# Performance work log

Measured on AMD Instinct MI355X. Metric: run time of the kernel, lower is better.

Reference implementation:

```python
import jax, jax.numpy as jnp
import numpy as np

N = 100000        # number of nodes
E = 3200000       # number of edges (avg degree 32)
D_IN = 128
D_OUT = 128


def setup_inputs() -> dict:
    key = jax.random.key(0)
    k_x, k_src, k_dst, k_w, k_W, k_b = jax.random.split(key, 6)
    x = jax.random.normal(k_x, (N, D_IN), dtype=jnp.float32)
    edge_src = jax.random.randint(k_src, (E,), 0, N, dtype=jnp.int32)
    edge_dst = jnp.sort(jax.random.randint(k_dst, (E,), 0, N, dtype=jnp.int32))
    edge_weight = jax.random.uniform(k_w, (E,), dtype=jnp.float32)
    # Linear params, init uniform(-stdv, stdv) with stdv = 1/sqrt(in_features)
    stdv = 1.0 / np.sqrt(D_IN)
    W = jax.random.uniform(k_W, (D_IN, D_OUT), dtype=jnp.float32, minval=-stdv, maxval=stdv)
    b = jax.random.uniform(k_b, (D_OUT,), dtype=jnp.float32, minval=-stdv, maxval=stdv)
    return {"x": x, "W": W, "b": b, "edge_weight": edge_weight,
            "edge_src": edge_src, "edge_dst": edge_dst}


def reference(x, W, b, edge_weight, edge_src, edge_dst):
    # support = W(input)  -- dense projection [N, D_OUT]
    support = x @ W + b
    # output = spmm(adj, support): out[dst] += w_e * support[src]
    msgs = support[edge_src] * edge_weight[:, None]          # [E, D_OUT]
    out = jax.ops.segment_sum(msgs, edge_dst, num_segments=x.shape[0])
    return out
```

## Files before the change

kernel.cpp:

```cpp
#include <hip/hip_runtime.h>

#define D 128

typedef unsigned short u16;
typedef __attribute__((ext_vector_type(8))) short bf16x8;
typedef __attribute__((ext_vector_type(4))) float f32x4;

__device__ __forceinline__ u16 f32_to_bf16(float f) {
    unsigned u = __float_as_uint(f);
    unsigned rounding = 0x7fffu + ((u >> 16) & 1u);
    return (u16)((u + rounding) >> 16);
}

__device__ __forceinline__ float bf16_to_f32(u16 s) {
    return __uint_as_float(((unsigned)s) << 16);
}

__global__ __launch_bounds__(256) void prep_kernel(
    const float* __restrict__ W, u16* __restrict__ Wt)
{
    int idx = blockIdx.x * 256 + threadIdx.x;
    int n = idx >> 7;
    int k = idx & 127;
    Wt[idx] = f32_to_bf16(W[k * 128 + n]);
}

__global__ __launch_bounds__(256) void gemm_mfma_kernel(
    const float* __restrict__ x, const u16* __restrict__ Wt,
    const float* __restrict__ b, u16* __restrict__ sup, int N)
{
    const int lane = threadIdx.x & 63;
    const int wave = threadIdx.x >> 6;
    const int col  = lane & 15;
    const int quad = lane >> 4;
    const int row0 = blockIdx.x * 64 + wave * 16;
    const int m    = row0 + col;
    const bool mvalid = (m < N);

    f32x4 acc[8];
    #pragma unroll
    for (int nt = 0; nt < 8; ++nt) {
        float bias = b[nt * 16 + col];
        acc[nt][0] = bias; acc[nt][1] = bias;
        acc[nt][2] = bias; acc[nt][3] = bias;
    }

    const float* xrow = x + (size_t)m * D;

    #pragma unroll
    for (int ks = 0; ks < 4; ++ks) {
        const int k0 = ks * 32 + quad * 8;

        float af[8];
        if (mvalid) {
            float4 v0 = *(const float4*)(xrow + k0);
            float4 v1 = *(const float4*)(xrow + k0 + 4);
            af[0] = v0.x; af[1] = v0.y; af[2] = v0.z; af[3] = v0.w;
            af[4] = v1.x; af[5] = v1.y; af[6] = v1.z; af[7] = v1.w;
        } else {
            #pragma unroll
            for (int j = 0; j < 8; ++j) af[j] = 0.f;
        }

        bf16x8 ahi, alo;
        #pragma unroll
        for (int j = 0; j < 8; ++j) {
            u16 h = f32_to_bf16(af[j]);
            float r = af[j] - bf16_to_f32(h);
            ahi[j] = (short)h;
            alo[j] = (short)f32_to_bf16(r);
        }

        #pragma unroll
        for (int nt = 0; nt < 8; ++nt) {
            bf16x8 bfrag = *(const bf16x8*)(Wt + (size_t)(nt * 16 + col) * D + k0);
            acc[nt] = __builtin_amdgcn_mfma_f32_16x16x32_bf16(alo, bfrag, acc[nt], 0, 0, 0);
            acc[nt] = __builtin_amdgcn_mfma_f32_16x16x32_bf16(ahi, bfrag, acc[nt], 0, 0, 0);
        }
    }

    #pragma unroll
    for (int reg = 0; reg < 4; ++reg) {
        int r = row0 + quad * 4 + reg;
        if (r < N) {
            #pragma unroll
            for (int nt = 0; nt < 8; ++nt) {
                sup[(size_t)r * D + nt * 16 + col] = f32_to_bf16(acc[nt][reg]);
            }
        }
    }
}

__global__ __launch_bounds__(256) void rowptr_kernel(
    const int* __restrict__ edst, int* __restrict__ rp, int E, int N)
{
    int e = blockIdx.x * 256 + threadIdx.x;
    if (e >= E) return;
    int d = edst[e];
    int prev = (e == 0) ? -1 : edst[e - 1];
    for (int n = prev + 1; n <= d; ++n) rp[n] = e;
    if (e == E - 1) {
        for (int n = d + 1; n <= N; ++n) rp[n] = E;
    }
}

__global__ __launch_bounds__(256) void spmm_kernel(
    const u16* __restrict__ sup, const float* __restrict__ ew,
    const int* __restrict__ esrc, const int* __restrict__ rp,
    float* __restrict__ out, int N)
{
    const int b    = blockIdx.x;
    const int xcd  = b & 7;
    const int half = xcd >> 2;
    const int grp  = (b >> 3) * 4 + (xcd & 3);
    const int wave = threadIdx.x >> 6;
    const int lane = threadIdx.x & 63;
    const int node = grp * 4 + wave;
    if (node >= N) return;

    const int start = rp[node];
    const int end   = rp[node + 1];

    const int eg = lane >> 3;
    const int fl = lane & 7;
    const unsigned off = (unsigned)half * 64u + (unsigned)fl * 8u;

    float acc[8];
    #pragma unroll
    for (int j = 0; j < 8; ++j) acc[j] = 0.f;

    for (int base = start; base < end; base += 64) {
        int cnt = end - base;
        if (cnt > 64) cnt = 64;

        int mi = base + lane;
        int   sv = (mi < end) ? esrc[mi] : 0;
        float wv = (mi < end) ? ew[mi]   : 0.f;

        for (int i = 0; i < cnt; i += 32) {
            uint4 u[4];
            float w[4];
            #pragma unroll
            for (int g = 0; g < 4; ++g) {
                int idx  = i + g * 8 + eg;
                int cidx = (idx < cnt) ? idx : (cnt - 1);
                int   s  = __shfl(sv, cidx);
                float wt = __shfl(wv, cidx);
                w[g] = (idx < cnt) ? wt : 0.f;
                u[g] = *(const uint4*)(sup + (size_t)s * D + off);
            }
            #pragma unroll
            for (int g = 0; g < 4; ++g) {
                unsigned d0 = u[g].x, d1 = u[g].y, d2 = u[g].z, d3 = u[g].w;
                acc[0] = fmaf(w[g], __uint_as_float(d0 << 16),         acc[0]);
                acc[1] = fmaf(w[g], __uint_as_float(d0 & 0xffff0000u), acc[1]);
                acc[2] = fmaf(w[g], __uint_as_float(d1 << 16),         acc[2]);
                acc[3] = fmaf(w[g], __uint_as_float(d1 & 0xffff0000u), acc[3]);
                acc[4] = fmaf(w[g], __uint_as_float(d2 << 16),         acc[4]);
                acc[5] = fmaf(w[g], __uint_as_float(d2 & 0xffff0000u), acc[5]);
                acc[6] = fmaf(w[g], __uint_as_float(d3 << 16),         acc[6]);
                acc[7] = fmaf(w[g], __uint_as_float(d3 & 0xffff0000u), acc[7]);
            }
        }
    }

    #pragma unroll
    for (int m = 8; m <= 32; m <<= 1) {
        #pragma unroll
        for (int j = 0; j < 8; ++j) acc[j] += __shfl_xor(acc[j], m);
    }

    if (eg == 0) {
        float* dst = out + (size_t)node * D + off;
        float4 o0 = make_float4(acc[0], acc[1], acc[2], acc[3]);
        float4 o1 = make_float4(acc[4], acc[5], acc[6], acc[7]);
        *(float4*)dst       = o0;
        *(float4*)(dst + 4) = o1;
    }
}

extern "C" void kernel_launch(void* const* d_in, const int* in_sizes, int n_in,
                              void* d_out, int out_size, void* d_ws, size_t ws_size,
                              hipStream_t stream) {
    const float* x    = (const float*)d_in[0];
    const float* W    = (const float*)d_in[1];
    const float* b    = (const float*)d_in[2];
    const float* ew   = (const float*)d_in[3];
    const int*   esrc = (const int*)d_in[4];
    const int*   edst = (const int*)d_in[5];
    float* out = (float*)d_out;

    const int N = in_sizes[0] / D;
    const int E = in_sizes[3];

    u16* sup = (u16*)d_ws;
    int* rp  = (int*)((char*)d_ws + (size_t)N * D * sizeof(u16));
    u16* Wt  = (u16*)((char*)rp + ((size_t)N + 16) * sizeof(int));

    hipLaunchKernelGGL(prep_kernel, dim3(64), dim3(256), 0, stream, W, Wt);
    hipLaunchKernelGGL(gemm_mfma_kernel, dim3((N + 63) / 64), dim3(256), 0, stream,
                       x, Wt, b, sup, N);
    hipLaunchKernelGGL(rowptr_kernel, dim3((E + 255) / 256), dim3(256), 0, stream,
                       edst, rp, E, N);

    int nblk_half = (N + 3) / 4;
    int grid_spmm = ((nblk_half + 3) / 4) * 8;
    hipLaunchKernelGGL(spmm_kernel, dim3(grid_spmm), dim3(256), 0, stream,
                       sup, ew, esrc, rp, out, N);
}
```

Baseline: 260.8 us.

## Map full feature row per wave in SpMM using readlane edge broadcast

Restructures the SpMM so each wave covers all 128 features of a node with 2 bf16 values per lane, iterating edges sequentially with scalar readlane broadcasts of source index and weight. This removes the cross-lane shuffle reduction and per-edge shuffles, and drops the XCD-aware split of feature halves. It trades wider per-lane vector loads and more edges in flight for narrower 4-byte loads, and may lose L2 locality from the XCD partitioning.

```diff
diff --git a/kernel.cpp b/kernel.cpp
--- a/kernel.cpp
+++ b/kernel.cpp
@@ -3,6 +3,7 @@
 #define D 128
 
 typedef unsigned short u16;
+typedef unsigned int   u32;
 typedef __attribute__((ext_vector_type(8))) short bf16x8;
 typedef __attribute__((ext_vector_type(4))) float f32x4;
 
@@ -109,74 +110,48 @@
     const int* __restrict__ esrc, const int* __restrict__ rp,
     float* __restrict__ out, int N)
 {
-    const int b    = blockIdx.x;
-    const int xcd  = b & 7;
-    const int half = xcd >> 2;
-    const int grp  = (b >> 3) * 4 + (xcd & 3);
     const int wave = threadIdx.x >> 6;
     const int lane = threadIdx.x & 63;
-    const int node = grp * 4 + wave;
+    const int node = blockIdx.x * 4 + wave;
     if (node >= N) return;
 
-    const int start = rp[node];
-    const int end   = rp[node + 1];
+    const int start = __builtin_amdgcn_readfirstlane(rp[node]);
+    const int end   = __builtin_amdgcn_readfirstlane(rp[node + 1]);
 
-    const int eg = lane >> 3;
-    const int fl = lane & 7;
-    const unsigned off = (unsigned)half * 64u + (unsigned)fl * 8u;
-
-    float acc[8];
-    #pragma unroll
-    for (int j = 0; j < 8; ++j) acc[j] = 0.f;
+    float acc0 = 0.f;
+    float acc1 = 0.f;
 
     for (int base = start; base < end; base += 64) {
-        int cnt = end - base;
-        if (cnt > 64) cnt = 64;
+        const int cnt = min(64, end - base);
+        const int mi  = base + lane;
+        int sv = 0;
+        int wv = 0;
+        if (mi < end) {
+            sv = esrc[mi];
+            wv = __float_as_int(ew[mi]);
+        }
 
-        int mi = base + lane;
-        int   sv = (mi < end) ? esrc[mi] : 0;
-        float wv = (mi < end) ? ew[mi]   : 0.f;
-
-        for (int i = 0; i < cnt; i += 32) {
-            uint4 u[4];
-            float w[4];
+        for (int i0 = 0; i0 < cnt; i0 += 8) {
+            u32 u[8];
+            float wf[8];
             #pragma unroll
-            for (int g = 0; g < 4; ++g) {
-                int idx  = i + g * 8 + eg;
-                int cidx = (idx < cnt) ? idx : (cnt - 1);
-                int   s  = __shfl(sv, cidx);
-                float wt = __shfl(wv, cidx);
-                w[g] = (idx < cnt) ? wt : 0.f;
-                u[g] = *(const uint4*)(sup + (size_t)s * D + off);
+            for (int t = 0; t < 8; ++t) {
+                int s  = __builtin_amdgcn_readlane(sv, i0 + t);
+                int wb = __builtin_amdgcn_readlane(wv, i0 + t);
+                const u32* prow = (const u32*)(sup + ((size_t)(u32)s << 7));
+                u[t]  = prow[lane];
+                wf[t] = __int_as_float(wb);
             }
             #pragma unroll
-            for (int g = 0; g < 4; ++g) {
-                unsigned d0 = u[g].x, d1 = u[g].y, d2 = u[g].z, d3 = u[g].w;
-                acc[0] = fmaf(w[g], __uint_as_float(d0 << 16),         acc[0]);
-                acc[1] = fmaf(w[g], __uint_as_float(d0 & 0xffff0000u), acc[1]);
-                acc[2] = fmaf(w[g], __uint_as_float(d1 << 16),         acc[2]);
-                acc[3] = fmaf(w[g], __uint_as_float(d1 & 0xffff0000u), acc[3]);
-                acc[4] = fmaf(w[g], __uint_as_float(d2 << 16),         acc[4]);
-                acc[5] = fmaf(w[g], __uint_as_float(d2 & 0xffff0000u), acc[5]);
-                acc[6] = fmaf(w[g], __uint_as_float(d3 << 16),         acc[6]);
-                acc[7] = fmaf(w[g], __uint_as_float(d3 & 0xffff0000u), acc[7]);
+            for (int t = 0; t < 8; ++t) {
+                acc0 = fmaf(wf[t], __uint_as_float(u[t] << 16),         acc0);
+                acc1 = fmaf(wf[t], __uint_as_float(u[t] & 0xffff0000u), acc1);
             }
         }
     }
 
-    #pragma unroll
-    for (int m = 8; m <= 32; m <<= 1) {
-        #pragma unroll
-        for (int j = 0; j < 8; ++j) acc[j] += __shfl_xor(acc[j], m);
-    }
-
-    if (eg == 0) {
-        float* dst = out + (size_t)node * D + off;
-        float4 o0 = make_float4(acc[0], acc[1], acc[2], acc[3]);
-        float4 o1 = make_float4(acc[4], acc[5], acc[6], acc[7]);
-        *(float4*)dst       = o0;
-        *(float4*)(dst + 4) = o1;
-    }
+    float2 o = make_float2(acc0, acc1);
+    *(float2*)(out + (size_t)node * D + lane * 2) = o;
 }
 
 extern "C" void kernel_launch(void* const* d_in, const int* in_sizes, int n_in,
@@ -203,8 +178,6 @@
     hipLaunchKernelGGL(rowptr_kernel, dim3((E + 255) / 256), dim3(256), 0, stream,
                        edst, rp, E, N);
 
-    int nblk_half = (N + 3) / 4;
-    int grid_spmm = ((nblk_half + 3) / 4) * 8;
-    hipLaunchKernelGGL(spmm_kernel, dim3(grid_spmm), dim3(256), 0, stream,
+    hipLaunchKernelGGL(spmm_kernel, dim3((N + 3) / 4), dim3(256), 0, stream,
                        sup, ew, esrc, rp, out, N);
 }
```

Result: slower. 270.1 us (+3.6%).

## Fuse all stages into one persistent kernel with software grid barriers

Applied to the files above, without the earlier changes.

Merges weight prep, row-pointer build, MFMA projection and CSR SpMM into a single persistent kernel of 512 blocks. Grid-wide atomic barriers separate the phases, replacing three extra kernel launches and their gaps. A memset resets the barrier counters. The SpMM inner loop now issues 8 gathers per batch instead of 4 to raise memory-level parallelism. Risks are deadlock if the 512 blocks are not all co-resident, and lower occupancy and less load balance from grid-stride loops with launch_bounds(256,2).

```diff
diff --git a/kernel.cpp b/kernel.cpp
--- a/kernel.cpp
+++ b/kernel.cpp
@@ -3,6 +3,7 @@
 #define D 128
 
 typedef unsigned short u16;
+typedef unsigned int   u32;
 typedef __attribute__((ext_vector_type(8))) short bf16x8;
 typedef __attribute__((ext_vector_type(4))) float f32x4;
 
@@ -16,166 +17,193 @@
     return __uint_as_float(((unsigned)s) << 16);
 }
 
-__global__ __launch_bounds__(256) void prep_kernel(
-    const float* __restrict__ W, u16* __restrict__ Wt)
+__device__ __forceinline__ void grid_barrier(int* ctr, int target) {
+    __syncthreads();
+    if (threadIdx.x == 0) {
+        __hip_atomic_fetch_add(ctr, 1, __ATOMIC_ACQ_REL, __HIP_MEMORY_SCOPE_AGENT);
+        while (__hip_atomic_load(ctr, __ATOMIC_ACQUIRE, __HIP_MEMORY_SCOPE_AGENT) < target) {
+            __builtin_amdgcn_s_sleep(2);
+        }
+    }
+    __syncthreads();
+}
+
+__global__ __launch_bounds__(256, 2) void fused_kernel(
+    const float* __restrict__ x, const float* __restrict__ W,
+    const float* __restrict__ b, const float* __restrict__ ew,
+    const int* __restrict__ esrc, const int* __restrict__ edst,
+    float* __restrict__ out, u16* __restrict__ sup,
+    int* __restrict__ rp, u16* __restrict__ Wt,
+    int* __restrict__ bar, int N, int E)
 {
-    int idx = blockIdx.x * 256 + threadIdx.x;
-    int n = idx >> 7;
-    int k = idx & 127;
-    Wt[idx] = f32_to_bf16(W[k * 128 + n]);
-}
-
-__global__ __launch_bounds__(256) void gemm_mfma_kernel(
-    const float* __restrict__ x, const u16* __restrict__ Wt,
-    const float* __restrict__ b, u16* __restrict__ sup, int N)
-{
-    const int lane = threadIdx.x & 63;
-    const int wave = threadIdx.x >> 6;
-    const int col  = lane & 15;
-    const int quad = lane >> 4;
-    const int row0 = blockIdx.x * 64 + wave * 16;
-    const int m    = row0 + col;
-    const bool mvalid = (m < N);
-
-    f32x4 acc[8];
-    #pragma unroll
-    for (int nt = 0; nt < 8; ++nt) {
-        float bias = b[nt * 16 + col];
-        acc[nt][0] = bias; acc[nt][1] = bias;
-        acc[nt][2] = bias; acc[nt][3] = bias;
-    }
-
-    const float* xrow = x + (size_t)m * D;
-
-    #pragma unroll
-    for (int ks = 0; ks < 4; ++ks) {
-        const int k0 = ks * 32 + quad * 8;
-
-        float af[8];
-        if (mvalid) {
-            float4 v0 = *(const float4*)(xrow + k0);
-            float4 v1 = *(const float4*)(xrow + k0 + 4);
-            af[0] = v0.x; af[1] = v0.y; af[2] = v0.z; af[3] = v0.w;
-            af[4] = v1.x; af[5] = v1.y; af[6] = v1.z; af[7] = v1.w;
-        } else {
-            #pragma unroll
-            for (int j = 0; j < 8; ++j) af[j] = 0.f;
-        }
-
-        bf16x8 ahi, alo;
-        #pragma unroll
-        for (int j = 0; j < 8; ++j) {
-            u16 h = f32_to_bf16(af[j]);
-            float r = af[j] - bf16_to_f32(h);
-            ahi[j] = (short)h;
-            alo[j] = (short)f32_to_bf16(r);
-        }
-
-        #pragma unroll
-        for (int nt = 0; nt < 8; ++nt) {
-            bf16x8 bfrag = *(const bf16x8*)(Wt + (size_t)(nt * 16 + col) * D + k0);
-            acc[nt] = __builtin_amdgcn_mfma_f32_16x16x32_bf16(alo, bfrag, acc[nt], 0, 0, 0);
-            acc[nt] = __builtin_amdgcn_mfma_f32_16x16x32_bf16(ahi, bfrag, acc[nt], 0, 0, 0);
-        }
-    }
-
-    #pragma unroll
-    for (int reg = 0; reg < 4; ++reg) {
-        int r = row0 + quad * 4 + reg;
-        if (r < N) {
+    const int tid  = threadIdx.x;
+    const int nblk = gridDim.x;
+
+    for (int vb = blockIdx.x; vb < 64; vb += nblk) {
+        int idx = vb * 256 + tid;
+        int n = idx >> 7;
+        int k = idx & 127;
+        Wt[idx] = f32_to_bf16(W[k * 128 + n]);
+    }
+
+    {
+        const int nvb = (E + 255) / 256;
+        for (int vb = blockIdx.x; vb < nvb; vb += nblk) {
+            int e = vb * 256 + tid;
+            if (e < E) {
+                int d = edst[e];
+                int prev = (e == 0) ? -1 : edst[e - 1];
+                for (int n = prev + 1; n <= d; ++n) rp[n] = e;
+                if (e == E - 1) {
+                    for (int n = d + 1; n <= N; ++n) rp[n] = E;
+                }
+            }
+        }
+    }
+
+    grid_barrier(bar, nblk);
+
+    {
+        const int lane = tid & 63;
+        const int wave = tid >> 6;
+        const int col  = lane & 15;
+        const int quad = lane >> 4;
+        const int nvb  = (N + 63) / 64;
+
+        for (int vb = blockIdx.x; vb < nvb; vb += nblk) {
+            const int row0 = vb * 64 + wave * 16;
+            const int m    = row0 + col;
+            const bool mvalid = (m < N);
+
+            f32x4 acc[8];
             #pragma unroll
             for (int nt = 0; nt < 8; ++nt) {
-                sup[(size_t)r * D + nt * 16 + col] = f32_to_bf16(acc[nt][reg]);
-            }
-        }
-    }
-}
-
-__global__ __launch_bounds__(256) void rowptr_kernel(
-    const int* __restrict__ edst, int* __restrict__ rp, int E, int N)
-{
-    int e = blockIdx.x * 256 + threadIdx.x;
-    if (e >= E) return;
-    int d = edst[e];
-    int prev = (e == 0) ? -1 : edst[e - 1];
-    for (int n = prev + 1; n <= d; ++n) rp[n] = e;
-    if (e == E - 1) {
-        for (int n = d + 1; n <= N; ++n) rp[n] = E;
-    }
-}
-
-__global__ __launch_bounds__(256) void spmm_kernel(
-    const u16* __restrict__ sup, const float* __restrict__ ew,
-    const int* __restrict__ esrc, const int* __restrict__ rp,
-    float* __restrict__ out, int N)
-{
-    const int b    = blockIdx.x;
-    const int xcd  = b & 7;
-    const int half = xcd >> 2;
-    const int grp  = (b >> 3) * 4 + (xcd & 3);
-    const int wave = threadIdx.x >> 6;
-    const int lane = threadIdx.x & 63;
-    const int node = grp * 4 + wave;
-    if (node >= N) return;
-
-    const int start = rp[node];
-    const int end   = rp[node + 1];
-
-    const int eg = lane >> 3;
-    const int fl = lane & 7;
-    const unsigned off = (unsigned)half * 64u + (unsigned)fl * 8u;
-
-    float acc[8];
-    #pragma unroll
-    for (int j = 0; j < 8; ++j) acc[j] = 0.f;
-
-    for (int base = start; base < end; base += 64) {
-        int cnt = end - base;
-        if (cnt > 64) cnt = 64;
-
-        int mi = base + lane;
-        int   sv = (mi < end) ? esrc[mi] : 0;
-        float wv = (mi < end) ? ew[mi]   : 0.f;
-
-        for (int i = 0; i < cnt; i += 32) {
-            uint4 u[4];
-            float w[4];
-            #pragma unroll
-            for (int g = 0; g < 4; ++g) {
-                int idx  = i + g * 8 + eg;
-                int cidx = (idx < cnt) ? idx : (cnt - 1);
-                int   s  = __shfl(sv, cidx);
-                float wt = __shfl(wv, cidx);
-                w[g] = (idx < cnt) ? wt : 0.f;
-                u[g] = *(const uint4*)(sup + (size_t)s * D + off);
-            }
-            #pragma unroll
-            for (int g = 0; g < 4; ++g) {
-                unsigned d0 = u[g].x, d1 = u[g].y, d2 = u[g].z, d3 = u[g].w;
-                acc[0] = fmaf(w[g], __uint_as_float(d0 << 16),         acc[0]);
-                acc[1] = fmaf(w[g], __uint_as_float(d0 & 0xffff0000u), acc[1]);
-                acc[2] = fmaf(w[g], __uint_as_float(d1 << 16),         acc[2]);
-                acc[3] = fmaf(w[g], __uint_as_float(d1 & 0xffff0000u), acc[3]);
-                acc[4] = fmaf(w[g], __uint_as_float(d2 << 16),         acc[4]);
-                acc[5] = fmaf(w[g], __uint_as_float(d2 & 0xffff0000u), acc[5]);
-                acc[6] = fmaf(w[g], __uint_as_float(d3 << 16),         acc[6]);
-                acc[7] = fmaf(w[g], __uint_as_float(d3 & 0xffff0000u), acc[7]);
-            }
-        }
-    }
-
-    #pragma unroll
-    for (int m = 8; m <= 32; m <<= 1) {
-        #pragma unroll
-        for (int j = 0; j < 8; ++j) acc[j] += __shfl_xor(acc[j], m);
-    }
-
-    if (eg == 0) {
-        float* dst = out + (size_t)node * D + off;
-        float4 o0 = make_float4(acc[0], acc[1], acc[2], acc[3]);
-        float4 o1 = make_float4(acc[4], acc[5], acc[6], acc[7]);
-        *(float4*)dst       = o0;
-        *(float4*)(dst + 4) = o1;
+                float bias = b[nt * 16 + col];
+                acc[nt][0] = bias; acc[nt][1] = bias;
+                acc[nt][2] = bias; acc[nt][3] = bias;
+            }
+
+            const float* xrow = x + (size_t)m * D;
+
+            #pragma unroll
+            for (int ks = 0; ks < 4; ++ks) {
+                const int k0 = ks * 32 + quad * 8;
+
+                float af[8];
+                if (mvalid) {
+                    float4 v0 = *(const float4*)(xrow + k0);
+                    float4 v1 = *(const float4*)(xrow + k0 + 4);
+                    af[0] = v0.x; af[1] = v0.y; af[2] = v0.z; af[3] = v0.w;
+                    af[4] = v1.x; af[5] = v1.y; af[6] = v1.z; af[7] = v1.w;
+                } else {
+                    #pragma unroll
+                    for (int j = 0; j < 8; ++j) af[j] = 0.f;
+                }
+
+                bf16x8 ahi, alo;
+                #pragma unroll
+                for (int j = 0; j < 8; ++j) {
+                    u16 h = f32_to_bf16(af[j]);
+                    float r = af[j] - bf16_to_f32(h);
+                    ahi[j] = (short)h;
+                    alo[j] = (short)f32_to_bf16(r);
+                }
+
+                #pragma unroll
+                for (int nt = 0; nt < 8; ++nt) {
+                    bf16x8 bfrag = *(const bf16x8*)(Wt + (size_t)(nt * 16 + col) * D + k0);
+                    acc[nt] = __builtin_amdgcn_mfma_f32_16x16x32_bf16(alo, bfrag, acc[nt], 0, 0, 0);
+                    acc[nt] = __builtin_amdgcn_mfma_f32_16x16x32_bf16(ahi, bfrag, acc[nt], 0, 0, 0);
+                }
+            }
+
+            #pragma unroll
+            for (int reg = 0; reg < 4; ++reg) {
+                int r = row0 + quad * 4 + reg;
+                if (r < N) {
+                    #pragma unroll
+                    for (int nt = 0; nt < 8; ++nt) {
+                        sup[(size_t)r * D + nt * 16 + col] = f32_to_bf16(acc[nt][reg]);
+                    }
+                }
+            }
+        }
+    }
+
+    grid_barrier(bar + 1, nblk);
+
+    {
+        const int wave = tid >> 6;
+        const int lane = tid & 63;
+        const int eg   = lane >> 3;
+        const int fl   = lane & 7;
+
+        const int nblk_half = (N + 3) / 4;
+        const int nvb = ((nblk_half + 3) / 4) * 8;
+
+        for (int vb = blockIdx.x; vb < nvb; vb += nblk) {
+            const int xcd  = vb & 7;
+            const int half = xcd >> 2;
+            const int grp  = (vb >> 3) * 4 + (xcd & 3);
+            const int node = grp * 4 + wave;
+            if (node >= N) continue;
+
+            const int start = rp[node];
+            const int end   = rp[node + 1];
+
+            const unsigned off = (unsigned)half * 64u + (unsigned)fl * 8u;
+
+            float acc[8];
+            #pragma unroll
+            for (int j = 0; j < 8; ++j) acc[j] = 0.f;
+
+            for (int base = start; base < end; base += 64) {
+                int cnt = end - base;
+                if (cnt > 64) cnt = 64;
+
+                int mi = base + lane;
+                int   sv = (mi < end) ? esrc[mi] : 0;
+                float wv = (mi < end) ? ew[mi]   : 0.f;
+
+                uint4 u[8];
+                float w[8];
+                #pragma unroll
+                for (int g = 0; g < 8; ++g) {
+                    int idx  = g * 8 + eg;
+                    int cidx = (idx < cnt) ? idx : (cnt - 1);
+                    int   s  = __shfl(sv, cidx);
+                    float wt = __shfl(wv, cidx);
+                    w[g] = (idx < cnt) ? wt : 0.f;
+                    u[g] = *(const uint4*)(sup + (size_t)s * D + off);
+                }
+                #pragma unroll
+                for (int g = 0; g < 8; ++g) {
+                    unsigned d0 = u[g].x, d1 = u[g].y, d2 = u[g].z, d3 = u[g].w;
+                    acc[0] = fmaf(w[g], __uint_as_float(d0 << 16),         acc[0]);
+                    acc[1] = fmaf(w[g], __uint_as_float(d0 & 0xffff0000u), acc[1]);
+                    acc[2] = fmaf(w[g], __uint_as_float(d1 << 16),         acc[2]);
+                    acc[3] = fmaf(w[g], __uint_as_float(d1 & 0xffff0000u), acc[3]);
+                    acc[4] = fmaf(w[g], __uint_as_float(d2 << 16),         acc[4]);
+                    acc[5] = fmaf(w[g], __uint_as_float(d2 & 0xffff0000u), acc[5]);
+                    acc[6] = fmaf(w[g], __uint_as_float(d3 << 16),         acc[6]);
+                    acc[7] = fmaf(w[g], __uint_as_float(d3 & 0xffff0000u), acc[7]);
+                }
+            }
+
+            #pragma unroll
+            for (int m = 8; m <= 32; m <<= 1) {
+                #pragma unroll
+                for (int j = 0; j < 8; ++j) acc[j] += __shfl_xor(acc[j], m);
+            }
+
+            if (eg == 0) {
+                float* dst = out + (size_t)node * D + off;
+                float4 o0 = make_float4(acc[0], acc[1], acc[2], acc[3]);
+                float4 o1 = make_float4(acc[4], acc[5], acc[6], acc[7]);
+                *(float4*)dst       = o0;
+                *(float4*)(dst + 4) = o1;
+            }
+        }
     }
 }
 
@@ -190,21 +218,16 @@
     const int*   edst = (const int*)d_in[5];
     float* out = (float*)d_out;
 
-    const int N = in_sizes[0] / D;
-    const int E = in_sizes[3];
+    int N = in_sizes[0] / D;
+    int E = in_sizes[3];
 
     u16* sup = (u16*)d_ws;
     int* rp  = (int*)((char*)d_ws + (size_t)N * D * sizeof(u16));
     u16* Wt  = (u16*)((char*)rp + ((size_t)N + 16) * sizeof(int));
-
-    hipLaunchKernelGGL(prep_kernel, dim3(64), dim3(256), 0, stream, W, Wt);
-    hipLaunchKernelGGL(gemm_mfma_kernel, dim3((N + 63) / 64), dim3(256), 0, stream,
-                       x, Wt, b, sup, N);
-    hipLaunchKernelGGL(rowptr_kernel, dim3((E + 255) / 256), dim3(256), 0, stream,
-                       edst, rp, E, N);
-
-    int nblk_half = (N + 3) / 4;
-    int grid_spmm = ((nblk_half + 3) / 4) * 8;
-    hipLaunchKernelGGL(spmm_kernel, dim3(grid_spmm), dim3(256), 0, stream,
-                       sup, ew, esrc, rp, out, N);
-}
+    int* bar = (int*)((char*)Wt + (size_t)128 * 128 * sizeof(u16));
+
+    hipMemsetAsync(bar, 0, 2 * sizeof(int), stream);
+
+    hipLaunchKernelGGL(fused_kernel, dim3(512), dim3(256), 0, stream,
+                       x, W, b, ew, esrc, edst, out, sup, rp, Wt, bar, N, E);
+}
```

Measured after the change: 434.8 us. 66.7% more time.

## Fuse W transpose, GEMM and rowptr build into one kernel with LDS-staged W

Applied to the files above, without the earlier changes.

Merges the weight-transpose prep, the MFMA GEMM and the row-pointer kernel into a single launch. Each block converts W to bf16 transposed into padded LDS, then runs the GEMM reading B fragments from LDS, then grid-strides over edge blocks to build the CSR row pointers. This removes two kernel launches and the global round trip for Wt. In exchange, every block repeats the 64KB W conversion, and the LDS footprint (about 34KB per block) may limit occupancy.

```diff
diff --git a/kernel.cpp b/kernel.cpp
--- a/kernel.cpp
+++ b/kernel.cpp
@@ -1,8 +1,10 @@
 #include <hip/hip_runtime.h>
 
 #define D 128
+#define WS 136
 
 typedef unsigned short u16;
+typedef unsigned int   u32;
 typedef __attribute__((ext_vector_type(8))) short bf16x8;
 typedef __attribute__((ext_vector_type(4))) float f32x4;
 
@@ -16,91 +18,100 @@
     return __uint_as_float(((unsigned)s) << 16);
 }
 
-__global__ __launch_bounds__(256) void prep_kernel(
-    const float* __restrict__ W, u16* __restrict__ Wt)
+__global__ __launch_bounds__(256) void gemm_rowptr_kernel(
+    const float* __restrict__ x, const float* __restrict__ W,
+    const float* __restrict__ b, const int* __restrict__ edst,
+    u16* __restrict__ sup, int* __restrict__ rp, int N, int E)
 {
-    int idx = blockIdx.x * 256 + threadIdx.x;
-    int n = idx >> 7;
-    int k = idx & 127;
-    Wt[idx] = f32_to_bf16(W[k * 128 + n]);
-}
-
-__global__ __launch_bounds__(256) void gemm_mfma_kernel(
-    const float* __restrict__ x, const u16* __restrict__ Wt,
-    const float* __restrict__ b, u16* __restrict__ sup, int N)
-{
-    const int lane = threadIdx.x & 63;
-    const int wave = threadIdx.x >> 6;
-    const int col  = lane & 15;
-    const int quad = lane >> 4;
-    const int row0 = blockIdx.x * 64 + wave * 16;
-    const int m    = row0 + col;
-    const bool mvalid = (m < N);
-
-    f32x4 acc[8];
+    __shared__ u16 Wt_lds[128 * WS];
+
+    const int tid = threadIdx.x;
+
     #pragma unroll
-    for (int nt = 0; nt < 8; ++nt) {
-        float bias = b[nt * 16 + col];
-        acc[nt][0] = bias; acc[nt][1] = bias;
-        acc[nt][2] = bias; acc[nt][3] = bias;
-    }
-
-    const float* xrow = x + (size_t)m * D;
-
-    #pragma unroll
-    for (int ks = 0; ks < 4; ++ks) {
-        const int k0 = ks * 32 + quad * 8;
-
-        float af[8];
-        if (mvalid) {
-            float4 v0 = *(const float4*)(xrow + k0);
-            float4 v1 = *(const float4*)(xrow + k0 + 4);
-            af[0] = v0.x; af[1] = v0.y; af[2] = v0.z; af[3] = v0.w;
-            af[4] = v1.x; af[5] = v1.y; af[6] = v1.z; af[7] = v1.w;
-        } else {
-            #pragma unroll
-            for (int j = 0; j < 8; ++j) af[j] = 0.f;
-        }
-
-        bf16x8 ahi, alo;
-        #pragma unroll
-        for (int j = 0; j < 8; ++j) {
-            u16 h = f32_to_bf16(af[j]);
-            float r = af[j] - bf16_to_f32(h);
-            ahi[j] = (short)h;
-            alo[j] = (short)f32_to_bf16(r);
-        }
-
+    for (int i = 0; i < 64; ++i) {
+        int idx = i * 256 + tid;
+        int k = idx >> 7;
+        int n = idx & 127;
+        Wt_lds[n * WS + k] = f32_to_bf16(W[idx]);
+    }
+    __syncthreads();
+
+    {
+        const int lane = tid & 63;
+        const int wave = tid >> 6;
+        const int col  = lane & 15;
+        const int quad = lane >> 4;
+        const int row0 = blockIdx.x * 64 + wave * 16;
+        const int m    = row0 + col;
+        const bool mvalid = (m < N);
+
+        f32x4 acc[8];
         #pragma unroll
         for (int nt = 0; nt < 8; ++nt) {
-            bf16x8 bfrag = *(const bf16x8*)(Wt + (size_t)(nt * 16 + col) * D + k0);
-            acc[nt] = __builtin_amdgcn_mfma_f32_16x16x32_bf16(alo, bfrag, acc[nt], 0, 0, 0);
-            acc[nt] = __builtin_amdgcn_mfma_f32_16x16x32_bf16(ahi, bfrag, acc[nt], 0, 0, 0);
-        }
-    }
-
-    #pragma unroll
-    for (int reg = 0; reg < 4; ++reg) {
-        int r = row0 + quad * 4 + reg;
-        if (r < N) {
+            float bias = b[nt * 16 + col];
+            acc[nt][0] = bias; acc[nt][1] = bias;
+            acc[nt][2] = bias; acc[nt][3] = bias;
+        }
+
+        const float* xrow = x + (size_t)m * D;
+
+        #pragma unroll
+        for (int ks = 0; ks < 4; ++ks) {
+            const int k0 = ks * 32 + quad * 8;
+
+            float af[8];
+            if (mvalid) {
+                float4 v0 = *(const float4*)(xrow + k0);
+                float4 v1 = *(const float4*)(xrow + k0 + 4);
+                af[0] = v0.x; af[1] = v0.y; af[2] = v0.z; af[3] = v0.w;
+                af[4] = v1.x; af[5] = v1.y; af[6] = v1.z; af[7] = v1.w;
+            } else {
+                #pragma unroll
+                for (int j = 0; j < 8; ++j) af[j] = 0.f;
+            }
+
+            bf16x8 ahi, alo;
+            #pragma unroll
+            for (int j = 0; j < 8; ++j) {
+                u16 h = f32_to_bf16(af[j]);
+                float r = af[j] - bf16_to_f32(h);
+                ahi[j] = (short)h;
+                alo[j] = (short)f32_to_bf16(r);
+            }
+
             #pragma unroll
             for (int nt = 0; nt < 8; ++nt) {
-                sup[(size_t)r * D + nt * 16 + col] = f32_to_bf16(acc[nt][reg]);
-            }
-        }
-    }
-}
-
-__global__ __launch_bounds__(256) void rowptr_kernel(
-    const int* __restrict__ edst, int* __restrict__ rp, int E, int N)
-{
-    int e = blockIdx.x * 256 + threadIdx.x;
-    if (e >= E) return;
-    int d = edst[e];
-    int prev = (e == 0) ? -1 : edst[e - 1];
-    for (int n = prev + 1; n <= d; ++n) rp[n] = e;
-    if (e == E - 1) {
-        for (int n = d + 1; n <= N; ++n) rp[n] = E;
+                bf16x8 bfrag = *(const bf16x8*)(&Wt_lds[(nt * 16 + col) * WS + k0]);
+                acc[nt] = __builtin_amdgcn_mfma_f32_16x16x32_bf16(alo, bfrag, acc[nt], 0, 0, 0);
+                acc[nt] = __builtin_amdgcn_mfma_f32_16x16x32_bf16(ahi, bfrag, acc[nt], 0, 0, 0);
+            }
+        }
+
+        #pragma unroll
+        for (int reg = 0; reg < 4; ++reg) {
+            int r = row0 + quad * 4 + reg;
+            if (r < N) {
+                #pragma unroll
+                for (int nt = 0; nt < 8; ++nt) {
+                    sup[(size_t)r * D + nt * 16 + col] = f32_to_bf16(acc[nt][reg]);
+                }
+            }
+        }
+    }
+
+    {
+        const int nvb = (E + 255) / 256;
+        for (int vb = blockIdx.x; vb < nvb; vb += gridDim.x) {
+            int e = vb * 256 + tid;
+            if (e < E) {
+                int d = edst[e];
+                int prev = (e == 0) ? -1 : edst[e - 1];
+                for (int n = prev + 1; n <= d; ++n) rp[n] = e;
+                if (e == E - 1) {
+                    for (int n = d + 1; n <= N; ++n) rp[n] = E;
+                }
+            }
+        }
     }
 }
 
@@ -195,13 +206,9 @@
 
     u16* sup = (u16*)d_ws;
     int* rp  = (int*)((char*)d_ws + (size_t)N * D * sizeof(u16));
-    u16* Wt  = (u16*)((char*)rp + ((size_t)N + 16) * sizeof(int));
-
-    hipLaunchKernelGGL(prep_kernel, dim3(64), dim3(256), 0, stream, W, Wt);
-    hipLaunchKernelGGL(gemm_mfma_kernel, dim3((N + 63) / 64), dim3(256), 0, stream,
-                       x, Wt, b, sup, N);
-    hipLaunchKernelGGL(rowptr_kernel, dim3((E + 255) / 256), dim3(256), 0, stream,
-                       edst, rp, E, N);
+
+    hipLaunchKernelGGL(gemm_rowptr_kernel, dim3((N + 63) / 64), dim3(256), 0, stream,
+                       x, W, b, edst, sup, rp, N, E);
 
     int nblk_half = (N + 3) / 4;
     int grid_spmm = ((nblk_half + 3) / 4) * 8;
```

After: 241.9 us, median of 2. 7.2% less time.
